# Performance work log

Measured on AMD Instinct MI355X. Metric: run time of the kernel, lower is better.

## Reference

```python
import jax, jax.numpy as jnp
import numpy as np

T, N, E = 4, 50000, 400000
F0, F1, F2 = 128, 128, 64


def _xavier(k, shape):
    a = float(np.sqrt(6.0 / (shape[0] + shape[1])))
    return jax.random.uniform(k, shape, jnp.float32, -a, a)


def setup_inputs() -> dict:
    key = jax.random.key(0)
    ks = jax.random.split(key, 32)
    inp = {
        'node_embs': jax.random.normal(ks[0], (T, N, F0), jnp.float32),
        'mask': jnp.zeros((T, N, 1), jnp.float32),
        'edge_src': jax.random.randint(ks[1], (T, E), 0, N, jnp.int32),
        'edge_dst': jax.random.randint(ks[2], (T, E), 0, N, jnp.int32),
        'edge_weight': jax.random.uniform(ks[3], (T, E), jnp.float32),
        'gcn_w0': _xavier(ks[4], (F0, F1)),
        'gcn_w1': _xavier(ks[5], (F1, F2)),
    }
    i = 6
    for (pre, rows, cols) in (('l0', F0, F1), ('l1', F1, F2)):
        for g in ('u', 'r', 'h'):
            inp[pre + '_W' + g] = _xavier(ks[i], (rows, rows)); i += 1
            inp[pre + '_U' + g] = _xavier(ks[i], (rows, rows)); i += 1
            inp[pre + '_B' + g] = jnp.zeros((rows, cols), jnp.float32)
        inp[pre + '_scorer'] = _xavier(ks[i], (rows, 1)); i += 1
    return inp


def _topk_embed(X, m, scorer, k):
    # scores: [N,1] = X @ scorer / ||scorer|| + mask
    scores = X @ scorer / jnp.linalg.norm(scorer) + m
    vals, idx = jax.lax.top_k(scores[:, 0], k)          # [k]
    return (X[idx] * jnp.tanh(vals)[:, None]).T         # [rows, k]


def _grcu(Q0, params, node_seq, mask_seq, src, dst, ew, k, n_nodes):
    Wu, Uu, Bu, Wr, Ur, Br, Wh, Uh, Bh, scorer = params

    def step(Q, xs):
        X, m, s, d, w = xs
        z = _topk_embed(X, m, scorer, k)                 # [rows, cols]
        upd = jax.nn.sigmoid(Wu @ z + Uu @ Q + Bu)
        rst = jax.nn.sigmoid(Wr @ z + Ur @ Q + Br)
        hcap = jnp.tanh(Wh @ z + Uh @ (rst * Q) + Bh)
        Qn = (1.0 - upd) * Q + upd * hcap                # evolved GCN weight
        XW = X @ Qn                                      # [N, cols]
        msg = XW[s] * w[:, None]                         # gather + scale
        out = jax.nn.relu(jax.ops.segment_sum(msg, d, num_segments=n_nodes))
        return Qn, out

    _, outs = jax.lax.scan(step, Q0, (node_seq, mask_seq, src, dst, ew))
    return outs  # [T, N, cols]


def reference(node_embs, mask, edge_src, edge_dst, edge_weight, gcn_w0, gcn_w1,
              l0_Wu, l0_Uu, l0_Bu, l0_Wr, l0_Ur, l0_Br, l0_Wh, l0_Uh, l0_Bh, l0_scorer,
              l1_Wu, l1_Uu, l1_Bu, l1_Wr, l1_Ur, l1_Br, l1_Wh, l1_Uh, l1_Bh, l1_scorer):
    p0 = (l0_Wu, l0_Uu, l0_Bu, l0_Wr, l0_Ur, l0_Br, l0_Wh, l0_Uh, l0_Bh, l0_scorer)
    p1 = (l1_Wu, l1_Uu, l1_Bu, l1_Wr, l1_Ur, l1_Br, l1_Wh, l1_Uh, l1_Bh, l1_scorer)
    n = node_embs.shape[1]
    h1 = _grcu(gcn_w0, p0, node_embs, mask, edge_src, edge_dst, edge_weight, gcn_w0.shape[1], n)
    h2 = _grcu(gcn_w1, p1, h1, mask, edge_src, edge_dst, edge_weight, gcn_w1.shape[1], n)
    return h2  # [T, N, F2]
```

## Files before the change

kernel.cpp:

```cpp
#include <hip/hip_runtime.h>
#include <math.h>

#define T_STEPS 4
#define NNODES 50000
#define NEDGES 400000
#define FIN 128
#define NBINS 8192
#define BINSHIFT 19
#define EQCAP 4096
#define DSHARD 6250

__device__ __forceinline__ float sigmoidf_(float x) { return 1.0f / (1.0f + __expf(-x)); }

__device__ __forceinline__ unsigned int key_of(float s) {
    unsigned int u = __float_as_uint(s);
    return (u & 0x80000000u) ? ~u : (u | 0x80000000u);
}

__device__ __forceinline__ unsigned short f2bf(float f) {
    unsigned int u = __float_as_uint(f);
    unsigned int r = (u + 0x7FFFu + ((u >> 16) & 1u)) >> 16;
    return (unsigned short)r;
}
__device__ __forceinline__ float bf2f(unsigned short h) {
    return __uint_as_float(((unsigned int)h) << 16);
}

__global__ void norm_kernel(const float* __restrict__ s0, const float* __restrict__ s1,
                            float* __restrict__ norms) {
    __shared__ float red[128];
    int tid = threadIdx.x;
    float a = s0[tid];
    red[tid] = a * a;
    __syncthreads();
    for (int off = 64; off > 0; off >>= 1) { if (tid < off) red[tid] += red[tid + off]; __syncthreads(); }
    if (tid == 0) norms[0] = sqrtf(red[0]);
    __syncthreads();
    float b = s1[tid];
    red[tid] = b * b;
    __syncthreads();
    for (int off = 64; off > 0; off >>= 1) { if (tid < off) red[tid] += red[tid + off]; __syncthreads(); }
    if (tid == 0) norms[1] = sqrtf(red[0]);
}

__global__ void scores_hist4_kernel(const float* __restrict__ node_embs, const float* __restrict__ scorer,
                                    const float* __restrict__ norms,
                                    const float* __restrict__ mask, float* __restrict__ scores4,
                                    int* __restrict__ ghist4, int N) {
    __shared__ float sc[FIN];
    if (threadIdx.x < FIN) sc[threadIdx.x] = scorer[threadIdx.x];
    __syncthreads();
    int t = blockIdx.y;
    int n = blockIdx.x * blockDim.x + threadIdx.x;
    if (n >= N) return;
    const float4* xr = (const float4*)(node_embs + ((size_t)t * N + n) * FIN);
    float acc = 0.f;
#pragma unroll 8
    for (int k4 = 0; k4 < FIN / 4; k4++) {
        float4 v = xr[k4];
        acc += v.x * sc[k4 * 4] + v.y * sc[k4 * 4 + 1] + v.z * sc[k4 * 4 + 2] + v.w * sc[k4 * 4 + 3];
    }
    float s = acc / norms[0] + mask[(size_t)t * N + n];
    scores4[(size_t)t * N + n] = s;
    atomicAdd(&ghist4[t * NBINS + (key_of(s) >> BINSHIFT)], 1);
}

__global__ void __launch_bounds__(256)
topk_collect_kernel(const float* __restrict__ scores_b, const int* __restrict__ ghist_b,
                    int* __restrict__ cnts_b, int* __restrict__ gt_idx_b, float* __restrict__ gt_val_b,
                    int* __restrict__ eq_idx_b, float* __restrict__ eq_val_b, int N, int K) {
    __shared__ int h[NBINS];
    __shared__ int part[256];
    __shared__ int s_bin;
    int tid = threadIdx.x;
    int task = blockIdx.y;
    const int* gh = ghist_b + (size_t)task * NBINS;
    for (int i = tid; i < NBINS; i += 256) h[i] = gh[i];
    __syncthreads();
    int s = 0;
#pragma unroll
    for (int i = 0; i < NBINS / 256; i++) s += h[tid * (NBINS / 256) + i];
    part[tid] = s;
    __syncthreads();
    for (int off = 1; off < 256; off <<= 1) {
        int v = (tid + off < 256) ? part[tid + off] : 0;
        __syncthreads();
        part[tid] += v;
        __syncthreads();
    }
    {
        int run = (tid == 255) ? 0 : part[tid + 1];
        const int CH = NBINS / 256;
        for (int b = tid * CH + CH - 1; b >= tid * CH; b--) {
            int Sb = run + h[b];
            if (Sb >= K && run < K) s_bin = b;
            run = Sb;
        }
    }
    __syncthreads();
    int bin = s_bin;
    const float* scores = scores_b + (size_t)task * N;
    int* cg = cnts_b + task * 2;
    for (int n = blockIdx.x * 256 + tid; n < N; n += gridDim.x * 256) {
        float sc = scores[n];
        unsigned int key = key_of(sc);
        int kb = (int)(key >> BINSHIFT);
        if (kb > bin) {
            int p = atomicAdd(&cg[0], 1);
            gt_idx_b[task * 128 + p] = n; gt_val_b[task * 128 + p] = sc;
        } else if (kb == bin) {
            int p = atomicAdd(&cg[1], 1);
            if (p < EQCAP) { eq_idx_b[task * EQCAP + p] = n; eq_val_b[task * EQCAP + p] = sc; }
        }
    }
}

template <int K>
__global__ void __launch_bounds__(1024)
topk_finish_kernel(int* __restrict__ ghist_b, int* __restrict__ cnts_b,
                   const int* __restrict__ gt_idx_b, const float* __restrict__ gt_val_b,
                   const int* __restrict__ eq_idx_b, const float* __restrict__ eq_val_b,
                   const float* __restrict__ X_b, float* __restrict__ z_b, int N) {
    __shared__ int sidx[K];
    __shared__ float sval[K];
    __shared__ unsigned int ek[EQCAP];
    __shared__ int ei[EQCAP];
    __shared__ int out_idx[K];
    __shared__ float out_tanh[K];
    int tid = threadIdx.x;
    int task = blockIdx.x;
    int* cg = cnts_b + task * 2;
    int g = cg[0];
    int m = min(cg[1], EQCAP);
    int need = K - g;
    const int* gt_idx = gt_idx_b + task * 128;
    const float* gt_val = gt_val_b + task * 128;
    const int* eq_idx = eq_idx_b + task * EQCAP;
    const float* eq_val = eq_val_b + task * EQCAP;
    const float* X = X_b + (size_t)task * N * FIN;
    float* z = z_b + (size_t)task * FIN * K;

    for (int i = tid; i < g; i += 1024) { sidx[i] = gt_idx[i]; sval[i] = gt_val[i]; }
    for (int i = tid; i < m; i += 1024) { ek[i] = key_of(eq_val[i]); ei[i] = eq_idx[i]; }
    __syncthreads();
    for (int i = tid; i < m; i += 1024) {
        int myi = ei[i];
        unsigned int myk = ek[i];
        int rank = 0;
        for (int j = 0; j < m; j++)
            rank += (ek[j] > myk) || (ek[j] == myk && ei[j] < myi);
        if (rank < need) { sidx[g + rank] = myi; sval[g + rank] = eq_val[i]; }
    }
    __syncthreads();
    if (tid < K) {
        float v = sval[tid];
        int id = sidx[tid];
        unsigned int myk = key_of(v);
        int rank = 0;
        for (int j = 0; j < K; j++) {
            unsigned int kj = key_of(sval[j]);
            rank += (kj > myk) || (kj == myk && sidx[j] < id);
        }
        out_idx[rank] = id;
        out_tanh[rank] = tanhf(v);
    }
    int* gh = ghist_b + (size_t)task * NBINS;
    for (int i = tid; i < NBINS; i += 1024) gh[i] = 0;
    if (tid == 0) { cg[0] = 0; cg[1] = 0; }
    __syncthreads();
    for (int i = tid; i < K * FIN; i += 1024) {
        int j = i >> 7;
        int r = i & 127;
        z[r * K + j] = X[(size_t)out_idx[j] * FIN + r] * out_tanh[j];
    }
}

template <int COLS>
__global__ void __launch_bounds__(256)
gru_multi_kernel(const float* __restrict__ Qinit, const float* __restrict__ z_all,
                 const float* __restrict__ Wu, const float* __restrict__ Uu, const float* __restrict__ Bu,
                 const float* __restrict__ Wr, const float* __restrict__ Ur, const float* __restrict__ Br,
                 const float* __restrict__ Wh, const float* __restrict__ Uh, const float* __restrict__ Bh,
                 float* __restrict__ Qn_all) {
    __shared__ float zc[128][8];
    __shared__ float qc[128][8];
    __shared__ float rq[128][8];
    __shared__ float ul[128][8];
    int tid = threadIdx.x;
    int c0 = blockIdx.x * 8;
    for (int i = tid; i < 1024; i += 256) {
        int r = i >> 3, c = i & 7;
        qc[r][c] = Qinit[r * COLS + c0 + c];
    }
    for (int t = 0; t < T_STEPS; t++) {
        __syncthreads();
        const float* z = z_all + (size_t)t * 128 * COLS;
        for (int i = tid; i < 1024; i += 256) {
            int r = i >> 3, c = i & 7;
            zc[r][c] = z[r * COLS + c0 + c];
        }
        __syncthreads();
#pragma unroll
        for (int e = 0; e < 4; e++) {
            int idx = tid + 256 * e;
            int r = idx >> 3, c = idx & 7;
            float au = Bu[r * COLS + c0 + c], ar = Br[r * COLS + c0 + c];
            for (int k = 0; k < 128; k++) {
                float zz = zc[k][c], qq = qc[k][c];
                au += Wu[r * 128 + k] * zz + Uu[r * 128 + k] * qq;
                ar += Wr[r * 128 + k] * zz + Ur[r * 128 + k] * qq;
            }
            ul[r][c] = sigmoidf_(au);
            rq[r][c] = sigmoidf_(ar) * qc[r][c];
        }
        __syncthreads();
        float* Qn = Qn_all + (size_t)t * 128 * COLS;
#pragma unroll
        for (int e = 0; e < 4; e++) {
            int idx = tid + 256 * e;
            int r = idx >> 3, c = idx & 7;
            float s = Bh[r * COLS + c0 + c];
            for (int k = 0; k < 128; k++) {
                s += Wh[r * 128 + k] * zc[k][c] + Uh[r * 128 + k] * rq[k][c];
            }
            float h = tanhf(s);
            float u = ul[r][c];
            float qn = (1.f - u) * qc[r][c] + u * h;
            Qn[r * COLS + c0 + c] = qn;
            qc[r][c] = qn;
        }
    }
}

template <int COLS, bool BF16>
__global__ void __launch_bounds__(256)
xw_kernel(const float* __restrict__ X_b, const float* __restrict__ Qn_all,
          void* __restrict__ outp, int N) {
    constexpr int TPR = COLS / 4;
    constexpr int RPG = 256 / TPR;
    constexpr int RPB = RPG * 4;
    int t = blockIdx.y;
    const float* X = X_b + (size_t)t * N * FIN;
    const float* Qn = Qn_all + (size_t)t * 128 * COLS;
    __shared__ float4 qs[128 * TPR];
    for (int i = threadIdx.x; i < 128 * TPR; i += 256) qs[i] = ((const float4*)Qn)[i];
    __syncthreads();
    int lane_c = threadIdx.x % TPR;
    int rloc = threadIdx.x / TPR;
    int base = blockIdx.x * RPB;
    int rows[4];
    float4 acc[4];
#pragma unroll
    for (int j = 0; j < 4; j++) {
        rows[j] = base + rloc + j * RPG;
        acc[j] = make_float4(0.f, 0.f, 0.f, 0.f);
    }
    int nc[4];
#pragma unroll
    for (int j = 0; j < 4; j++) nc[j] = min(rows[j], N - 1);

    for (int k4 = 0; k4 < 32; k4++) {
        float4 q0 = qs[(k4 * 4 + 0) * TPR + lane_c];
        float4 q1 = qs[(k4 * 4 + 1) * TPR + lane_c];
        float4 q2 = qs[(k4 * 4 + 2) * TPR + lane_c];
        float4 q3 = qs[(k4 * 4 + 3) * TPR + lane_c];
#pragma unroll
        for (int j = 0; j < 4; j++) {
            float4 xv = ((const float4*)(X + (size_t)nc[j] * FIN))[k4];
            acc[j].x += xv.x * q0.x + xv.y * q1.x + xv.z * q2.x + xv.w * q3.x;
            acc[j].y += xv.x * q0.y + xv.y * q1.y + xv.z * q2.y + xv.w * q3.y;
            acc[j].z += xv.x * q0.z + xv.y * q1.z + xv.z * q2.z + xv.w * q3.z;
            acc[j].w += xv.x * q0.w + xv.y * q1.w + xv.z * q2.w + xv.w * q3.w;
        }
    }
#pragma unroll
    for (int j = 0; j < 4; j++) {
        if (rows[j] < N) {
            if (BF16) {
                ushort4 o;
                o.x = f2bf(acc[j].x); o.y = f2bf(acc[j].y);
                o.z = f2bf(acc[j].z); o.w = f2bf(acc[j].w);
                ((ushort4*)((unsigned short*)outp + ((size_t)t * N + rows[j]) * COLS))[lane_c] = o;
            } else {
                ((float4*)((float*)outp + ((size_t)t * N + rows[j]) * COLS))[lane_c] = acc[j];
            }
        }
    }
}

__global__ void hist4_kernel(const int* __restrict__ dst, int* __restrict__ hist4, int E) {
    int e = blockIdx.x * blockDim.x + threadIdx.x;
    if (e >= E) return;
    int t = blockIdx.y;
    atomicAdd(&hist4[t * NNODES + dst[(size_t)t * E + e]], 1);
}

__global__ void __launch_bounds__(256)
scanA_kernel(const int* __restrict__ hist, int* __restrict__ incl, int* __restrict__ bsum, int M) {
    __shared__ int sh[256];
    int gid = blockIdx.x * 256 + threadIdx.x;
    int v = (gid < M) ? hist[gid] : 0;
    sh[threadIdx.x] = v;
    __syncthreads();
    for (int off = 1; off < 256; off <<= 1) {
        int u = (threadIdx.x >= off) ? sh[threadIdx.x - off] : 0;
        __syncthreads();
        sh[threadIdx.x] += u;
        __syncthreads();
    }
    if (gid < M) incl[gid] = sh[threadIdx.x];
    if (threadIdx.x == 255) bsum[blockIdx.x] = sh[255];
}

__global__ void __launch_bounds__(1024)
scanB_kernel(int* __restrict__ bsum, int nb) {
    __shared__ int sh[1024];
    int tid = threadIdx.x;
    int v = (tid < nb) ? bsum[tid] : 0;
    sh[tid] = v;
    __syncthreads();
    for (int off = 1; off < 1024; off <<= 1) {
        int u = (tid >= off) ? sh[tid - off] : 0;
        __syncthreads();
        sh[tid] += u;
        __syncthreads();
    }
    if (tid < nb) bsum[tid] = (tid == 0) ? 0 : sh[tid - 1];
}

__global__ void __launch_bounds__(256)
scanC_kernel(const int* __restrict__ hist, const int* __restrict__ incl,
             const int* __restrict__ bsum, int* __restrict__ row_ptr,
             int* __restrict__ cursor, int M) {
    int gid = blockIdx.x * 256 + threadIdx.x;
    if (gid < M) {
        int inc = incl[gid] + bsum[gid / 256];
        int ex = inc - hist[gid];
        row_ptr[gid] = ex;
        cursor[gid] = ex;
        if (gid == M - 1) row_ptr[M] = inc;
    }
}

__global__ void bucket4_kernel(const int* __restrict__ src, const int* __restrict__ dst,
                               const float* __restrict__ w, int* __restrict__ cursor,
                               int2* __restrict__ sedge, int E) {
    int bx = blockIdx.x;
    int shard = bx & 7;
    int e = (bx >> 3) * 256 + threadIdx.x;
    if (e >= E) return;
    int t = blockIdx.y;
    size_t ge = (size_t)t * E + e;
    int d = dst[ge];
    if (d / DSHARD != shard) return;
    int pos = atomicAdd(&cursor[t * NNODES + d], 1);
    int2 pk;
    pk.x = src[ge];
    pk.y = __float_as_int(w[ge]);
    sedge[pos] = pk;
}

template <int COLS, bool SCORE, bool BF16>
__global__ void __launch_bounds__(256)
agg_kernel(const void* __restrict__ XWp, const int* __restrict__ row_ptr4,
           const int2* __restrict__ sedge,
           float* __restrict__ out_b, int N,
           const float* __restrict__ scorer, const float* __restrict__ norms,
           const float* __restrict__ mask_b, float* __restrict__ scores_b, int* __restrict__ ghist_b) {
    constexpr int TPN = COLS / 4;
    constexpr int NPB = 256 / TPN;
    int t = blockIdx.y;
    int node = blockIdx.x * NPB + threadIdx.x / TPN;
    int lane = threadIdx.x % TPN;
    if (node >= N) return;
    const int* rp = row_ptr4 + (size_t)t * N;
    int beg = rp[node], end = rp[node + 1];
    size_t xwoff = (size_t)t * N * COLS;
    float4 a0 = make_float4(0.f, 0.f, 0.f, 0.f);
    float4 a1 = a0, a2 = a0, a3 = a0;
    int i = beg;
    for (; i + 4 <= end; i += 4) {
        int2 p0 = sedge[i], p1 = sedge[i + 1], p2 = sedge[i + 2], p3 = sedge[i + 3];
        if (BF16) {
            const unsigned short* XW = (const unsigned short*)XWp + xwoff;
            ushort4 v0 = ((const ushort4*)(XW + (size_t)p0.x * COLS))[lane];
            ushort4 v1 = ((const ushort4*)(XW + (size_t)p1.x * COLS))[lane];
            ushort4 v2 = ((const ushort4*)(XW + (size_t)p2.x * COLS))[lane];
            ushort4 v3 = ((const ushort4*)(XW + (size_t)p3.x * COLS))[lane];
            float w0 = __int_as_float(p0.y), w1 = __int_as_float(p1.y);
            float w2 = __int_as_float(p2.y), w3 = __int_as_float(p3.y);
            a0.x += bf2f(v0.x) * w0; a0.y += bf2f(v0.y) * w0; a0.z += bf2f(v0.z) * w0; a0.w += bf2f(v0.w) * w0;
            a1.x += bf2f(v1.x) * w1; a1.y += bf2f(v1.y) * w1; a1.z += bf2f(v1.z) * w1; a1.w += bf2f(v1.w) * w1;
            a2.x += bf2f(v2.x) * w2; a2.y += bf2f(v2.y) * w2; a2.z += bf2f(v2.z) * w2; a2.w += bf2f(v2.w) * w2;
            a3.x += bf2f(v3.x) * w3; a3.y += bf2f(v3.y) * w3; a3.z += bf2f(v3.z) * w3; a3.w += bf2f(v3.w) * w3;
        } else {
            const float* XW = (const float*)XWp + xwoff;
            float4 v0 = ((const float4*)(XW + (size_t)p0.x * COLS))[lane];
            float4 v1 = ((const float4*)(XW + (size_t)p1.x * COLS))[lane];
            float4 v2 = ((const float4*)(XW + (size_t)p2.x * COLS))[lane];
            float4 v3 = ((const float4*)(XW + (size_t)p3.x * COLS))[lane];
            float w0 = __int_as_float(p0.y), w1 = __int_as_float(p1.y);
            float w2 = __int_as_float(p2.y), w3 = __int_as_float(p3.y);
            a0.x += v0.x * w0; a0.y += v0.y * w0; a0.z += v0.z * w0; a0.w += v0.w * w0;
            a1.x += v1.x * w1; a1.y += v1.y * w1; a1.z += v1.z * w1; a1.w += v1.w * w1;
            a2.x += v2.x * w2; a2.y += v2.y * w2; a2.z += v2.z * w2; a2.w += v2.w * w2;
            a3.x += v3.x * w3; a3.y += v3.y * w3; a3.z += v3.z * w3; a3.w += v3.w * w3;
        }
    }
    for (; i < end; i++) {
        int2 pk = sedge[i];
        float wt = __int_as_float(pk.y);
        if (BF16) {
            const unsigned short* XW = (const unsigned short*)XWp + xwoff;
            ushort4 v = ((const ushort4*)(XW + (size_t)pk.x * COLS))[lane];
            a0.x += bf2f(v.x) * wt; a0.y += bf2f(v.y) * wt;
            a0.z += bf2f(v.z) * wt; a0.w += bf2f(v.w) * wt;
        } else {
            const float* XW = (const float*)XWp + xwoff;
            float4 v = ((const float4*)(XW + (size_t)pk.x * COLS))[lane];
            a0.x += v.x * wt; a0.y += v.y * wt; a0.z += v.z * wt; a0.w += v.w * wt;
        }
    }
    float4 acc;
    acc.x = (a0.x + a1.x) + (a2.x + a3.x);
    acc.y = (a0.y + a1.y) + (a2.y + a3.y);
    acc.z = (a0.z + a1.z) + (a2.z + a3.z);
    acc.w = (a0.w + a1.w) + (a2.w + a3.w);
    acc.x = fmaxf(acc.x, 0.f); acc.y = fmaxf(acc.y, 0.f);
    acc.z = fmaxf(acc.z, 0.f); acc.w = fmaxf(acc.w, 0.f);
    ((float4*)(out_b + ((size_t)t * N + node) * COLS))[lane] = acc;
    if (SCORE) {
        float4 sc4 = ((const float4*)scorer)[lane];
        float partial = acc.x * sc4.x + acc.y * sc4.y + acc.z * sc4.z + acc.w * sc4.w;
#pragma unroll
        for (int off = TPN / 2; off > 0; off >>= 1) partial += __shfl_xor(partial, off, TPN);
        if (lane == 0) {
            float s = partial / norms[1] + mask_b[(size_t)t * N + node];
            scores_b[(size_t)t * N + node] = s;
            atomicAdd(&ghist_b[t * NBINS + (key_of(s) >> BINSHIFT)], 1);
        }
    }
}

extern "C" void kernel_launch(void* const* d_in, const int* in_sizes, int n_in,
                              void* d_out, int out_size, void* d_ws, size_t ws_size,
                              hipStream_t stream) {
    const float* node_embs   = (const float*)d_in[0];
    const float* mask        = (const float*)d_in[1];
    const int*   edge_src    = (const int*)d_in[2];
    const int*   edge_dst    = (const int*)d_in[3];
    const float* edge_weight = (const float*)d_in[4];
    const float* gcn_w0      = (const float*)d_in[5];
    const float* gcn_w1      = (const float*)d_in[6];
    const float* l0p[10];
    const float* l1p[10];
    for (int i = 0; i < 10; i++) l0p[i] = (const float*)d_in[7 + i];
    for (int i = 0; i < 10; i++) l1p[i] = (const float*)d_in[17 + i];

    char* ws = (char*)d_ws;
    size_t off = 0;
    auto alloc = [&](size_t bytes) -> void* {
        void* p = ws + off;
        off += (bytes + 255) / 256 * 256;
        return p;
    };
    float* XW0buf = (float*)alloc((size_t)4 * NNODES * 128 * 4);
    float* h1buf  = (float*)alloc((size_t)4 * NNODES * 128 * 4);
    unsigned short* XW1buf = (unsigned short*)alloc((size_t)4 * NNODES * 64 * 2);
    float* scores4= (float*)alloc((size_t)4 * NNODES * 4);
    float* scores1= (float*)alloc((size_t)4 * NNODES * 4);
    float* z0buf  = (float*)alloc((size_t)4 * 128 * 128 * 4);
    float* z1buf  = (float*)alloc((size_t)4 * 128 * 64 * 4);
    float* Q0n    = (float*)alloc((size_t)4 * 128 * 128 * 4);
    float* Q1n    = (float*)alloc((size_t)4 * 128 * 64 * 4);
    float* norms  = (float*)alloc(64);
    int* hist4    = (int*)alloc(((size_t)4 * NNODES + 8 * NBINS + 64) * 4);
    int* ghist0   = hist4 + 4 * NNODES;
    int* ghist1   = ghist0 + 4 * NBINS;
    int* cnts     = ghist1 + 4 * NBINS;
    int* incl4    = (int*)alloc((size_t)4 * NNODES * 4);
    int* bsumb    = (int*)alloc(1024 * 4);
    int* rowp4    = (int*)alloc(((size_t)4 * NNODES + 1) * 4);
    int* cursor4  = (int*)alloc((size_t)4 * NNODES * 4);
    int2* sedge4  = (int2*)alloc((size_t)4 * NEDGES * 8);
    int*   gt_idx = (int*)alloc((size_t)4 * 128 * 4);
    float* gt_val = (float*)alloc((size_t)4 * 128 * 4);
    int*   eq_idx = (int*)alloc((size_t)4 * EQCAP * 4);
    float* eq_val = (float*)alloc((size_t)4 * EQCAP * 4);

    hipMemsetAsync(hist4, 0, ((size_t)4 * NNODES + 8 * NBINS + 64) * 4, stream);
    norm_kernel<<<1, 128, 0, stream>>>(l0p[9], l1p[9], norms);

    const int M4 = 4 * NNODES;
    const int NB4 = (M4 + 255) / 256;
    const int NB = (NNODES + 255) / 256;
    const int EB = (NEDGES + 255) / 256;

    hist4_kernel<<<dim3(EB, 4), 256, 0, stream>>>(edge_dst, hist4, NEDGES);
    scanA_kernel<<<NB4, 256, 0, stream>>>(hist4, incl4, bsumb, M4);
    scanB_kernel<<<1, 1024, 0, stream>>>(bsumb, NB4);
    scanC_kernel<<<NB4, 256, 0, stream>>>(hist4, incl4, bsumb, rowp4, cursor4, M4);
    bucket4_kernel<<<dim3(EB * 8, 4), 256, 0, stream>>>(edge_src, edge_dst, edge_weight, cursor4, sedge4, NEDGES);

    scores_hist4_kernel<<<dim3(NB, 4), 256, 0, stream>>>(node_embs, l0p[9], norms, mask, scores4, ghist0, NNODES);
    topk_collect_kernel<<<dim3(NB, 4), 256, 0, stream>>>(scores4, ghist0, cnts, gt_idx, gt_val, eq_idx, eq_val, NNODES, 128);
    topk_finish_kernel<128><<<4, 1024, 0, stream>>>(ghist0, cnts, gt_idx, gt_val, eq_idx, eq_val, node_embs, z0buf, NNODES);

    gru_multi_kernel<128><<<16, 256, 0, stream>>>(gcn_w0, z0buf,
        l0p[0], l0p[1], l0p[2], l0p[3], l0p[4], l0p[5], l0p[6], l0p[7], l0p[8], Q0n);
    xw_kernel<128, false><<<dim3((NNODES + 31) / 32, 4), 256, 0, stream>>>(node_embs, Q0n, XW0buf, NNODES);
    agg_kernel<128, true, false><<<dim3((NNODES + 7) / 8, 4), 256, 0, stream>>>(XW0buf, rowp4, sedge4, h1buf, NNODES,
        l1p[9], norms, mask, scores1, ghist1);

    topk_collect_kernel<<<dim3(NB, 4), 256, 0, stream>>>(scores1, ghist1, cnts, gt_idx, gt_val, eq_idx, eq_val, NNODES, 64);
    topk_finish_kernel<64><<<4, 1024, 0, stream>>>(ghist1, cnts, gt_idx, gt_val, eq_idx, eq_val, h1buf, z1buf, NNODES);
    gru_multi_kernel<64><<<8, 256, 0, stream>>>(gcn_w1, z1buf,
        l1p[0], l1p[1], l1p[2], l1p[3], l1p[4], l1p[5], l1p[6], l1p[7], l1p[8], Q1n);
    xw_kernel<64, true><<<dim3((NNODES + 63) / 64, 4), 256, 0, stream>>>(h1buf, Q1n, XW1buf, NNODES);
    agg_kernel<64, false, true><<<dim3((NNODES + 15) / 16, 4), 256, 0, stream>>>(XW1buf, rowp4, sedge4, (float*)d_out, NNODES,
        nullptr, nullptr, nullptr, nullptr, nullptr);
}
```

Baseline: 1.229 ms.

## Shard CSR edges by source range and map aggregation blocks to XCDs

Edges for each (timestep, destination) are now grouped into 8 source-range shards, using a larger histogram and a two-level prefix scan. The aggregation kernel walks the shards in order, with a block barrier after each one, so concurrently running blocks gather from the same slice of XW and that slice can stay resident in L2. Block indices are also remapped so that each pair of XCDs works on a single timestep. The cost is an 8x larger histogram, scan and cursor workspace, an extra scan pass, per-shard loop overhead and barriers, and very short per-shard edge runs that mostly fall into the non-unrolled tail loop.

```diff
diff --git a/kernel.cpp b/kernel.cpp
--- a/kernel.cpp
+++ b/kernel.cpp
@@ -288,11 +288,14 @@
     }
 }
 
-__global__ void hist4_kernel(const int* __restrict__ dst, int* __restrict__ hist4, int E) {
+__global__ void hist8_kernel(const int* __restrict__ src, const int* __restrict__ dst,
+                             int* __restrict__ hist8, int E) {
     int e = blockIdx.x * blockDim.x + threadIdx.x;
     if (e >= E) return;
     int t = blockIdx.y;
-    atomicAdd(&hist4[t * NNODES + dst[(size_t)t * E + e]], 1);
+    size_t ge = (size_t)t * E + e;
+    int s = src[ge] / DSHARD;
+    atomicAdd(&hist8[(t * 8 + s) * NNODES + dst[ge]], 1);
 }
 
 __global__ void __launch_bounds__(256)
@@ -329,12 +332,15 @@
 }
 
 __global__ void __launch_bounds__(256)
-scanC_kernel(const int* __restrict__ hist, const int* __restrict__ incl,
-             const int* __restrict__ bsum, int* __restrict__ row_ptr,
-             int* __restrict__ cursor, int M) {
+scanC2_kernel(const int* __restrict__ hist, const int* __restrict__ inclA,
+              const int* __restrict__ bsumA, const int* __restrict__ inclB,
+              const int* __restrict__ bsumB, int* __restrict__ row_ptr,
+              int* __restrict__ cursor, int M) {
     int gid = blockIdx.x * 256 + threadIdx.x;
     if (gid < M) {
-        int inc = incl[gid] + bsum[gid / 256];
+        int b = gid >> 8;
+        int exBlock = inclB[b] - bsumA[b] + bsumB[b >> 8];
+        int inc = inclA[gid] + exBlock;
         int ex = inc - hist[gid];
         row_ptr[gid] = ex;
         cursor[gid] = ex;
@@ -342,7 +348,7 @@
     }
 }
 
-__global__ void bucket4_kernel(const int* __restrict__ src, const int* __restrict__ dst,
+__global__ void bucket8_kernel(const int* __restrict__ src, const int* __restrict__ dst,
                                const float* __restrict__ w, int* __restrict__ cursor,
                                int2* __restrict__ sedge, int E) {
     int bx = blockIdx.x;
@@ -351,75 +357,85 @@
     if (e >= E) return;
     int t = blockIdx.y;
     size_t ge = (size_t)t * E + e;
+    int sc = src[ge];
+    if (sc / DSHARD != shard) return;
     int d = dst[ge];
-    if (d / DSHARD != shard) return;
-    int pos = atomicAdd(&cursor[t * NNODES + d], 1);
+    int pos = atomicAdd(&cursor[(t * 8 + shard) * NNODES + d], 1);
     int2 pk;
-    pk.x = src[ge];
+    pk.x = sc;
     pk.y = __float_as_int(w[ge]);
     sedge[pos] = pk;
 }
 
 template <int COLS, bool SCORE, bool BF16>
 __global__ void __launch_bounds__(256)
-agg_kernel(const void* __restrict__ XWp, const int* __restrict__ row_ptr4,
+agg_kernel(const void* __restrict__ XWp, const int* __restrict__ rp8,
            const int2* __restrict__ sedge,
            float* __restrict__ out_b, int N,
            const float* __restrict__ scorer, const float* __restrict__ norms,
            const float* __restrict__ mask_b, float* __restrict__ scores_b, int* __restrict__ ghist_b) {
     constexpr int TPN = COLS / 4;
     constexpr int NPB = 256 / TPN;
-    int t = blockIdx.y;
-    int node = blockIdx.x * NPB + threadIdx.x / TPN;
+    int lin = blockIdx.x;
+    int xcd = lin & 7;
+    int slot = lin >> 3;
+    int t = xcd >> 1;
+    int db = slot * 2 + (xcd & 1);
+    int dstBlocks = (N + NPB - 1) / NPB;
+    if (db >= dstBlocks) return;
+    int node = db * NPB + threadIdx.x / TPN;
     int lane = threadIdx.x % TPN;
-    if (node >= N) return;
-    const int* rp = row_ptr4 + (size_t)t * N;
-    int beg = rp[node], end = rp[node + 1];
     size_t xwoff = (size_t)t * N * COLS;
     float4 a0 = make_float4(0.f, 0.f, 0.f, 0.f);
     float4 a1 = a0, a2 = a0, a3 = a0;
-    int i = beg;
-    for (; i + 4 <= end; i += 4) {
-        int2 p0 = sedge[i], p1 = sedge[i + 1], p2 = sedge[i + 2], p3 = sedge[i + 3];
-        if (BF16) {
-            const unsigned short* XW = (const unsigned short*)XWp + xwoff;
-            ushort4 v0 = ((const ushort4*)(XW + (size_t)p0.x * COLS))[lane];
-            ushort4 v1 = ((const ushort4*)(XW + (size_t)p1.x * COLS))[lane];
-            ushort4 v2 = ((const ushort4*)(XW + (size_t)p2.x * COLS))[lane];
-            ushort4 v3 = ((const ushort4*)(XW + (size_t)p3.x * COLS))[lane];
-            float w0 = __int_as_float(p0.y), w1 = __int_as_float(p1.y);
-            float w2 = __int_as_float(p2.y), w3 = __int_as_float(p3.y);
-            a0.x += bf2f(v0.x) * w0; a0.y += bf2f(v0.y) * w0; a0.z += bf2f(v0.z) * w0; a0.w += bf2f(v0.w) * w0;
-            a1.x += bf2f(v1.x) * w1; a1.y += bf2f(v1.y) * w1; a1.z += bf2f(v1.z) * w1; a1.w += bf2f(v1.w) * w1;
-            a2.x += bf2f(v2.x) * w2; a2.y += bf2f(v2.y) * w2; a2.z += bf2f(v2.z) * w2; a2.w += bf2f(v2.w) * w2;
-            a3.x += bf2f(v3.x) * w3; a3.y += bf2f(v3.y) * w3; a3.z += bf2f(v3.z) * w3; a3.w += bf2f(v3.w) * w3;
-        } else {
-            const float* XW = (const float*)XWp + xwoff;
-            float4 v0 = ((const float4*)(XW + (size_t)p0.x * COLS))[lane];
-            float4 v1 = ((const float4*)(XW + (size_t)p1.x * COLS))[lane];
-            float4 v2 = ((const float4*)(XW + (size_t)p2.x * COLS))[lane];
-            float4 v3 = ((const float4*)(XW + (size_t)p3.x * COLS))[lane];
-            float w0 = __int_as_float(p0.y), w1 = __int_as_float(p1.y);
-            float w2 = __int_as_float(p2.y), w3 = __int_as_float(p3.y);
-            a0.x += v0.x * w0; a0.y += v0.y * w0; a0.z += v0.z * w0; a0.w += v0.w * w0;
-            a1.x += v1.x * w1; a1.y += v1.y * w1; a1.z += v1.z * w1; a1.w += v1.w * w1;
-            a2.x += v2.x * w2; a2.y += v2.y * w2; a2.z += v2.z * w2; a2.w += v2.w * w2;
-            a3.x += v3.x * w3; a3.y += v3.y * w3; a3.z += v3.z * w3; a3.w += v3.w * w3;
-        }
-    }
-    for (; i < end; i++) {
-        int2 pk = sedge[i];
-        float wt = __int_as_float(pk.y);
-        if (BF16) {
-            const unsigned short* XW = (const unsigned short*)XWp + xwoff;
-            ushort4 v = ((const ushort4*)(XW + (size_t)pk.x * COLS))[lane];
-            a0.x += bf2f(v.x) * wt; a0.y += bf2f(v.y) * wt;
-            a0.z += bf2f(v.z) * wt; a0.w += bf2f(v.w) * wt;
-        } else {
-            const float* XW = (const float*)XWp + xwoff;
-            float4 v = ((const float4*)(XW + (size_t)pk.x * COLS))[lane];
-            a0.x += v.x * wt; a0.y += v.y * wt; a0.z += v.z * wt; a0.w += v.w * wt;
-        }
+#pragma unroll 1
+    for (int s = 0; s < 8; s++) {
+        size_t ridx = (size_t)(t * 8 + s) * N + node;
+        int i = rp8[ridx];
+        int end = rp8[ridx + 1];
+        for (; i + 4 <= end; i += 4) {
+            int2 p0 = sedge[i], p1 = sedge[i + 1], p2 = sedge[i + 2], p3 = sedge[i + 3];
+            if (BF16) {
+                const unsigned short* XW = (const unsigned short*)XWp + xwoff;
+                ushort4 v0 = ((const ushort4*)(XW + (size_t)p0.x * COLS))[lane];
+                ushort4 v1 = ((const ushort4*)(XW + (size_t)p1.x * COLS))[lane];
+                ushort4 v2 = ((const ushort4*)(XW + (size_t)p2.x * COLS))[lane];
+                ushort4 v3 = ((const ushort4*)(XW + (size_t)p3.x * COLS))[lane];
+                float w0 = __int_as_float(p0.y), w1 = __int_as_float(p1.y);
+                float w2 = __int_as_float(p2.y), w3 = __int_as_float(p3.y);
+                a0.x += bf2f(v0.x) * w0; a0.y += bf2f(v0.y) * w0; a0.z += bf2f(v0.z) * w0; a0.w += bf2f(v0.w) * w0;
+                a1.x += bf2f(v1.x) * w1; a1.y += bf2f(v1.y) * w1; a1.z += bf2f(v1.z) * w1; a1.w += bf2f(v1.w) * w1;
+                a2.x += bf2f(v2.x) * w2; a2.y += bf2f(v2.y) * w2; a2.z += bf2f(v2.z) * w2; a2.w += bf2f(v2.w) * w2;
+                a3.x += bf2f(v3.x) * w3; a3.y += bf2f(v3.y) * w3; a3.z += bf2f(v3.z) * w3; a3.w += bf2f(v3.w) * w3;
+            } else {
+                const float* XW = (const float*)XWp + xwoff;
+                float4 v0 = ((const float4*)(XW + (size_t)p0.x * COLS))[lane];
+                float4 v1 = ((const float4*)(XW + (size_t)p1.x * COLS))[lane];
+                float4 v2 = ((const float4*)(XW + (size_t)p2.x * COLS))[lane];
+                float4 v3 = ((const float4*)(XW + (size_t)p3.x * COLS))[lane];
+                float w0 = __int_as_float(p0.y), w1 = __int_as_float(p1.y);
+                float w2 = __int_as_float(p2.y), w3 = __int_as_float(p3.y);
+                a0.x += v0.x * w0; a0.y += v0.y * w0; a0.z += v0.z * w0; a0.w += v0.w * w0;
+                a1.x += v1.x * w1; a1.y += v1.y * w1; a1.z += v1.z * w1; a1.w += v1.w * w1;
+                a2.x += v2.x * w2; a2.y += v2.y * w2; a2.z += v2.z * w2; a2.w += v2.w * w2;
+                a3.x += v3.x * w3; a3.y += v3.y * w3; a3.z += v3.z * w3; a3.w += v3.w * w3;
+            }
+        }
+        for (; i < end; i++) {
+            int2 pk = sedge[i];
+            float wt = __int_as_float(pk.y);
+            if (BF16) {
+                const unsigned short* XW = (const unsigned short*)XWp + xwoff;
+                ushort4 v = ((const ushort4*)(XW + (size_t)pk.x * COLS))[lane];
+                a0.x += bf2f(v.x) * wt; a0.y += bf2f(v.y) * wt;
+                a0.z += bf2f(v.z) * wt; a0.w += bf2f(v.w) * wt;
+            } else {
+                const float* XW = (const float*)XWp + xwoff;
+                float4 v = ((const float4*)(XW + (size_t)pk.x * COLS))[lane];
+                a0.x += v.x * wt; a0.y += v.y * wt; a0.z += v.z * wt; a0.w += v.w * wt;
+            }
+        }
+        __syncthreads();
     }
     float4 acc;
     acc.x = (a0.x + a1.x) + (a2.x + a3.x);
@@ -474,33 +490,37 @@
     float* Q0n    = (float*)alloc((size_t)4 * 128 * 128 * 4);
     float* Q1n    = (float*)alloc((size_t)4 * 128 * 64 * 4);
     float* norms  = (float*)alloc(64);
-    int* hist4    = (int*)alloc(((size_t)4 * NNODES + 8 * NBINS + 64) * 4);
-    int* ghist0   = hist4 + 4 * NNODES;
+    const int M8 = 32 * NNODES;
+    int* hist8    = (int*)alloc(((size_t)M8 + 8 * NBINS + 64) * 4);
+    int* ghist0   = hist8 + M8;
     int* ghist1   = ghist0 + 4 * NBINS;
     int* cnts     = ghist1 + 4 * NBINS;
-    int* incl4    = (int*)alloc((size_t)4 * NNODES * 4);
-    int* bsumb    = (int*)alloc(1024 * 4);
-    int* rowp4    = (int*)alloc(((size_t)4 * NNODES + 1) * 4);
-    int* cursor4  = (int*)alloc((size_t)4 * NNODES * 4);
+    int* inclA    = (int*)alloc((size_t)M8 * 4);
+    int* bsumA    = (int*)alloc(8192 * 4);
+    int* inclB    = (int*)alloc(8192 * 4);
+    int* bsumB    = (int*)alloc(1024 * 4);
+    int* rowp8    = (int*)alloc(((size_t)M8 + 1) * 4);
+    int* cursor8  = (int*)alloc((size_t)M8 * 4);
     int2* sedge4  = (int2*)alloc((size_t)4 * NEDGES * 8);
     int*   gt_idx = (int*)alloc((size_t)4 * 128 * 4);
     float* gt_val = (float*)alloc((size_t)4 * 128 * 4);
     int*   eq_idx = (int*)alloc((size_t)4 * EQCAP * 4);
     float* eq_val = (float*)alloc((size_t)4 * EQCAP * 4);
 
-    hipMemsetAsync(hist4, 0, ((size_t)4 * NNODES + 8 * NBINS + 64) * 4, stream);
+    hipMemsetAsync(hist8, 0, ((size_t)M8 + 8 * NBINS + 64) * 4, stream);
     norm_kernel<<<1, 128, 0, stream>>>(l0p[9], l1p[9], norms);
 
-    const int M4 = 4 * NNODES;
-    const int NB4 = (M4 + 255) / 256;
     const int NB = (NNODES + 255) / 256;
     const int EB = (NEDGES + 255) / 256;
-
-    hist4_kernel<<<dim3(EB, 4), 256, 0, stream>>>(edge_dst, hist4, NEDGES);
-    scanA_kernel<<<NB4, 256, 0, stream>>>(hist4, incl4, bsumb, M4);
-    scanB_kernel<<<1, 1024, 0, stream>>>(bsumb, NB4);
-    scanC_kernel<<<NB4, 256, 0, stream>>>(hist4, incl4, bsumb, rowp4, cursor4, M4);
-    bucket4_kernel<<<dim3(EB * 8, 4), 256, 0, stream>>>(edge_src, edge_dst, edge_weight, cursor4, sedge4, NEDGES);
+    const int NB8  = (M8 + 255) / 256;
+    const int NB8b = (NB8 + 255) / 256;
+
+    hist8_kernel<<<dim3(EB, 4), 256, 0, stream>>>(edge_src, edge_dst, hist8, NEDGES);
+    scanA_kernel<<<NB8, 256, 0, stream>>>(hist8, inclA, bsumA, M8);
+    scanA_kernel<<<NB8b, 256, 0, stream>>>(bsumA, inclB, bsumB, NB8);
+    scanB_kernel<<<1, 1024, 0, stream>>>(bsumB, NB8b);
+    scanC2_kernel<<<NB8, 256, 0, stream>>>(hist8, inclA, bsumA, inclB, bsumB, rowp8, cursor8, M8);
+    bucket8_kernel<<<dim3(EB * 8, 4), 256, 0, stream>>>(edge_src, edge_dst, edge_weight, cursor8, sedge4, NEDGES);
 
     scores_hist4_kernel<<<dim3(NB, 4), 256, 0, stream>>>(node_embs, l0p[9], norms, mask, scores4, ghist0, NNODES);
     topk_collect_kernel<<<dim3(NB, 4), 256, 0, stream>>>(scores4, ghist0, cnts, gt_idx, gt_val, eq_idx, eq_val, NNODES, 128);
@@ -509,14 +529,22 @@
     gru_multi_kernel<128><<<16, 256, 0, stream>>>(gcn_w0, z0buf,
         l0p[0], l0p[1], l0p[2], l0p[3], l0p[4], l0p[5], l0p[6], l0p[7], l0p[8], Q0n);
     xw_kernel<128, false><<<dim3((NNODES + 31) / 32, 4), 256, 0, stream>>>(node_embs, Q0n, XW0buf, NNODES);
-    agg_kernel<128, true, false><<<dim3((NNODES + 7) / 8, 4), 256, 0, stream>>>(XW0buf, rowp4, sedge4, h1buf, NNODES,
-        l1p[9], norms, mask, scores1, ghist1);
+    {
+        const int dstBlocks0 = (NNODES + 7) / 8;
+        const int grid0 = ((dstBlocks0 + 1) / 2) * 8;
+        agg_kernel<128, true, false><<<grid0, 256, 0, stream>>>(XW0buf, rowp8, sedge4, h1buf, NNODES,
+            l1p[9], norms, mask, scores1, ghist1);
+    }
 
     topk_collect_kernel<<<dim3(NB, 4), 256, 0, stream>>>(scores1, ghist1, cnts, gt_idx, gt_val, eq_idx, eq_val, NNODES, 64);
     topk_finish_kernel<64><<<4, 1024, 0, stream>>>(ghist1, cnts, gt_idx, gt_val, eq_idx, eq_val, h1buf, z1buf, NNODES);
     gru_multi_kernel<64><<<8, 256, 0, stream>>>(gcn_w1, z1buf,
         l1p[0], l1p[1], l1p[2], l1p[3], l1p[4], l1p[5], l1p[6], l1p[7], l1p[8], Q1n);
     xw_kernel<64, true><<<dim3((NNODES + 63) / 64, 4), 256, 0, stream>>>(h1buf, Q1n, XW1buf, NNODES);
-    agg_kernel<64, false, true><<<dim3((NNODES + 15) / 16, 4), 256, 0, stream>>>(XW1buf, rowp4, sedge4, (float*)d_out, NNODES,
-        nullptr, nullptr, nullptr, nullptr, nullptr);
-}
+    {
+        const int dstBlocks1 = (NNODES + 15) / 16;
+        const int grid1 = ((dstBlocks1 + 1) / 2) * 8;
+        agg_kernel<64, false, true><<<grid1, 256, 0, stream>>>(XW1buf, rowp8, sedge4, (float*)d_out, NNODES,
+            nullptr, nullptr, nullptr, nullptr, nullptr);
+    }
+}
```

Result: slower. 1.324 ms (+7.7%).

## Split layer-0 aggregation into column-slice passes with XCD-aware block mapping

Applied to the files above, without the earlier changes.

The layer-0 gather-aggregate runs as four passes, each over a 32-column slice of XW, so the gathered working set per pass (50000×32 floats per timestep) is more likely to stay cache-resident. Partial scorer dot products carry across passes in a new scoreacc buffer. Both aggregation kernels remap the flat block index so each XCD (index mod 8) handles one timestep's half of the destinations, keeping that timestep's XW in that XCD's L2. Outputs use nontemporal stores. The cost is re-reading the CSR edge list four times and three extra launches.

```diff
diff --git a/kernel.cpp b/kernel.cpp
--- a/kernel.cpp
+++ b/kernel.cpp
@@ -24,6 +24,12 @@
 }
 __device__ __forceinline__ float bf2f(unsigned short h) {
     return __uint_as_float(((unsigned int)h) << 16);
+}
+
+typedef float f4v __attribute__((ext_vector_type(4)));
+__device__ __forceinline__ void nt_store4(float* p, float4 v) {
+    f4v w; w.x = v.x; w.y = v.y; w.z = v.z; w.w = v.w;
+    __builtin_nontemporal_store(w, (f4v*)p);
 }
 
 __global__ void norm_kernel(const float* __restrict__ s0, const float* __restrict__ s1,
@@ -360,66 +366,51 @@
     sedge[pos] = pk;
 }
 
-template <int COLS, bool SCORE, bool BF16>
-__global__ void __launch_bounds__(256)
-agg_kernel(const void* __restrict__ XWp, const int* __restrict__ row_ptr4,
-           const int2* __restrict__ sedge,
-           float* __restrict__ out_b, int N,
-           const float* __restrict__ scorer, const float* __restrict__ norms,
-           const float* __restrict__ mask_b, float* __restrict__ scores_b, int* __restrict__ ghist_b) {
-    constexpr int TPN = COLS / 4;
+template <int SW, bool SCORE>
+__global__ void __launch_bounds__(256)
+agg_slice_kernel(const float* __restrict__ XW_b, const int* __restrict__ row_ptr4,
+                 const int2* __restrict__ sedge,
+                 float* __restrict__ out_b, int N, int P,
+                 const float* __restrict__ scorer, const float* __restrict__ norms,
+                 const float* __restrict__ mask_b, float* __restrict__ scores_b,
+                 int* __restrict__ ghist_b, float* __restrict__ scoreacc) {
+    constexpr int TPN = SW / 4;
     constexpr int NPB = 256 / TPN;
-    int t = blockIdx.y;
-    int node = blockIdx.x * NPB + threadIdx.x / TPN;
+    constexpr int NPASS = FIN / SW;
+    int lin = blockIdx.x;
+    int xcd = lin & 7;
+    int slot = lin >> 3;
+    int t = xcd >> 1;
+    int db = slot * 2 + (xcd & 1);
+    int dstBlocks = (N + NPB - 1) / NPB;
+    if (db >= dstBlocks) return;
+    int node = db * NPB + threadIdx.x / TPN;
+    if (node >= N) return;
     int lane = threadIdx.x % TPN;
-    if (node >= N) return;
     const int* rp = row_ptr4 + (size_t)t * N;
     int beg = rp[node], end = rp[node + 1];
-    size_t xwoff = (size_t)t * N * COLS;
+    const float* XW = XW_b + (size_t)t * N * FIN + P * SW;
     float4 a0 = make_float4(0.f, 0.f, 0.f, 0.f);
     float4 a1 = a0, a2 = a0, a3 = a0;
     int i = beg;
     for (; i + 4 <= end; i += 4) {
         int2 p0 = sedge[i], p1 = sedge[i + 1], p2 = sedge[i + 2], p3 = sedge[i + 3];
-        if (BF16) {
-            const unsigned short* XW = (const unsigned short*)XWp + xwoff;
-            ushort4 v0 = ((const ushort4*)(XW + (size_t)p0.x * COLS))[lane];
-            ushort4 v1 = ((const ushort4*)(XW + (size_t)p1.x * COLS))[lane];
-            ushort4 v2 = ((const ushort4*)(XW + (size_t)p2.x * COLS))[lane];
-            ushort4 v3 = ((const ushort4*)(XW + (size_t)p3.x * COLS))[lane];
-            float w0 = __int_as_float(p0.y), w1 = __int_as_float(p1.y);
-            float w2 = __int_as_float(p2.y), w3 = __int_as_float(p3.y);
-            a0.x += bf2f(v0.x) * w0; a0.y += bf2f(v0.y) * w0; a0.z += bf2f(v0.z) * w0; a0.w += bf2f(v0.w) * w0;
-            a1.x += bf2f(v1.x) * w1; a1.y += bf2f(v1.y) * w1; a1.z += bf2f(v1.z) * w1; a1.w += bf2f(v1.w) * w1;
-            a2.x += bf2f(v2.x) * w2; a2.y += bf2f(v2.y) * w2; a2.z += bf2f(v2.z) * w2; a2.w += bf2f(v2.w) * w2;
-            a3.x += bf2f(v3.x) * w3; a3.y += bf2f(v3.y) * w3; a3.z += bf2f(v3.z) * w3; a3.w += bf2f(v3.w) * w3;
-        } else {
-            const float* XW = (const float*)XWp + xwoff;
-            float4 v0 = ((const float4*)(XW + (size_t)p0.x * COLS))[lane];
-            float4 v1 = ((const float4*)(XW + (size_t)p1.x * COLS))[lane];
-            float4 v2 = ((const float4*)(XW + (size_t)p2.x * COLS))[lane];
-            float4 v3 = ((const float4*)(XW + (size_t)p3.x * COLS))[lane];
-            float w0 = __int_as_float(p0.y), w1 = __int_as_float(p1.y);
-            float w2 = __int_as_float(p2.y), w3 = __int_as_float(p3.y);
-            a0.x += v0.x * w0; a0.y += v0.y * w0; a0.z += v0.z * w0; a0.w += v0.w * w0;
-            a1.x += v1.x * w1; a1.y += v1.y * w1; a1.z += v1.z * w1; a1.w += v1.w * w1;
-            a2.x += v2.x * w2; a2.y += v2.y * w2; a2.z += v2.z * w2; a2.w += v2.w * w2;
-            a3.x += v3.x * w3; a3.y += v3.y * w3; a3.z += v3.z * w3; a3.w += v3.w * w3;
-        }
+        float4 v0 = ((const float4*)(XW + (size_t)p0.x * FIN))[lane];
+        float4 v1 = ((const float4*)(XW + (size_t)p1.x * FIN))[lane];
+        float4 v2 = ((const float4*)(XW + (size_t)p2.x * FIN))[lane];
+        float4 v3 = ((const float4*)(XW + (size_t)p3.x * FIN))[lane];
+        float w0 = __int_as_float(p0.y), w1 = __int_as_float(p1.y);
+        float w2 = __int_as_float(p2.y), w3 = __int_as_float(p3.y);
+        a0.x += v0.x * w0; a0.y += v0.y * w0; a0.z += v0.z * w0; a0.w += v0.w * w0;
+        a1.x += v1.x * w1; a1.y += v1.y * w1; a1.z += v1.z * w1; a1.w += v1.w * w1;
+        a2.x += v2.x * w2; a2.y += v2.y * w2; a2.z += v2.z * w2; a2.w += v2.w * w2;
+        a3.x += v3.x * w3; a3.y += v3.y * w3; a3.z += v3.z * w3; a3.w += v3.w * w3;
     }
     for (; i < end; i++) {
         int2 pk = sedge[i];
         float wt = __int_as_float(pk.y);
-        if (BF16) {
-            const unsigned short* XW = (const unsigned short*)XWp + xwoff;
-            ushort4 v = ((const ushort4*)(XW + (size_t)pk.x * COLS))[lane];
-            a0.x += bf2f(v.x) * wt; a0.y += bf2f(v.y) * wt;
-            a0.z += bf2f(v.z) * wt; a0.w += bf2f(v.w) * wt;
-        } else {
-            const float* XW = (const float*)XWp + xwoff;
-            float4 v = ((const float4*)(XW + (size_t)pk.x * COLS))[lane];
-            a0.x += v.x * wt; a0.y += v.y * wt; a0.z += v.z * wt; a0.w += v.w * wt;
-        }
+        float4 v = ((const float4*)(XW + (size_t)pk.x * FIN))[lane];
+        a0.x += v.x * wt; a0.y += v.y * wt; a0.z += v.z * wt; a0.w += v.w * wt;
     }
     float4 acc;
     acc.x = (a0.x + a1.x) + (a2.x + a3.x);
@@ -428,18 +419,77 @@
     acc.w = (a0.w + a1.w) + (a2.w + a3.w);
     acc.x = fmaxf(acc.x, 0.f); acc.y = fmaxf(acc.y, 0.f);
     acc.z = fmaxf(acc.z, 0.f); acc.w = fmaxf(acc.w, 0.f);
-    ((float4*)(out_b + ((size_t)t * N + node) * COLS))[lane] = acc;
+    nt_store4(out_b + ((size_t)t * N + node) * FIN + P * SW + lane * 4, acc);
     if (SCORE) {
-        float4 sc4 = ((const float4*)scorer)[lane];
+        float4 sc4 = ((const float4*)(scorer + P * SW))[lane];
         float partial = acc.x * sc4.x + acc.y * sc4.y + acc.z * sc4.z + acc.w * sc4.w;
 #pragma unroll
         for (int off = TPN / 2; off > 0; off >>= 1) partial += __shfl_xor(partial, off, TPN);
         if (lane == 0) {
-            float s = partial / norms[1] + mask_b[(size_t)t * N + node];
-            scores_b[(size_t)t * N + node] = s;
-            atomicAdd(&ghist_b[t * NBINS + (key_of(s) >> BINSHIFT)], 1);
-        }
-    }
+            float* sa = scoreacc + (size_t)t * N + node;
+            float tot = (P == 0 ? 0.f : *sa) + partial;
+            if (P == NPASS - 1) {
+                float s = tot / norms[1] + mask_b[(size_t)t * N + node];
+                scores_b[(size_t)t * N + node] = s;
+                atomicAdd(&ghist_b[t * NBINS + (key_of(s) >> BINSHIFT)], 1);
+            } else {
+                *sa = tot;
+            }
+        }
+    }
+}
+
+template <int COLS>
+__global__ void __launch_bounds__(256)
+agg_kernel(const unsigned short* __restrict__ XWb, const int* __restrict__ row_ptr4,
+           const int2* __restrict__ sedge,
+           float* __restrict__ out_b, int N) {
+    constexpr int TPN = COLS / 4;
+    constexpr int NPB = 256 / TPN;
+    int lin = blockIdx.x;
+    int xcd = lin & 7;
+    int slot = lin >> 3;
+    int t = xcd >> 1;
+    int db = slot * 2 + (xcd & 1);
+    int dstBlocks = (N + NPB - 1) / NPB;
+    if (db >= dstBlocks) return;
+    int node = db * NPB + threadIdx.x / TPN;
+    if (node >= N) return;
+    int lane = threadIdx.x % TPN;
+    const int* rp = row_ptr4 + (size_t)t * N;
+    int beg = rp[node], end = rp[node + 1];
+    const unsigned short* XW = XWb + (size_t)t * N * COLS;
+    float4 a0 = make_float4(0.f, 0.f, 0.f, 0.f);
+    float4 a1 = a0, a2 = a0, a3 = a0;
+    int i = beg;
+    for (; i + 4 <= end; i += 4) {
+        int2 p0 = sedge[i], p1 = sedge[i + 1], p2 = sedge[i + 2], p3 = sedge[i + 3];
+        ushort4 v0 = ((const ushort4*)(XW + (size_t)p0.x * COLS))[lane];
+        ushort4 v1 = ((const ushort4*)(XW + (size_t)p1.x * COLS))[lane];
+        ushort4 v2 = ((const ushort4*)(XW + (size_t)p2.x * COLS))[lane];
+        ushort4 v3 = ((const ushort4*)(XW + (size_t)p3.x * COLS))[lane];
+        float w0 = __int_as_float(p0.y), w1 = __int_as_float(p1.y);
+        float w2 = __int_as_float(p2.y), w3 = __int_as_float(p3.y);
+        a0.x += bf2f(v0.x) * w0; a0.y += bf2f(v0.y) * w0; a0.z += bf2f(v0.z) * w0; a0.w += bf2f(v0.w) * w0;
+        a1.x += bf2f(v1.x) * w1; a1.y += bf2f(v1.y) * w1; a1.z += bf2f(v1.z) * w1; a1.w += bf2f(v1.w) * w1;
+        a2.x += bf2f(v2.x) * w2; a2.y += bf2f(v2.y) * w2; a2.z += bf2f(v2.z) * w2; a2.w += bf2f(v2.w) * w2;
+        a3.x += bf2f(v3.x) * w3; a3.y += bf2f(v3.y) * w3; a3.z += bf2f(v3.z) * w3; a3.w += bf2f(v3.w) * w3;
+    }
+    for (; i < end; i++) {
+        int2 pk = sedge[i];
+        float wt = __int_as_float(pk.y);
+        ushort4 v = ((const ushort4*)(XW + (size_t)pk.x * COLS))[lane];
+        a0.x += bf2f(v.x) * wt; a0.y += bf2f(v.y) * wt;
+        a0.z += bf2f(v.z) * wt; a0.w += bf2f(v.w) * wt;
+    }
+    float4 acc;
+    acc.x = (a0.x + a1.x) + (a2.x + a3.x);
+    acc.y = (a0.y + a1.y) + (a2.y + a3.y);
+    acc.z = (a0.z + a1.z) + (a2.z + a3.z);
+    acc.w = (a0.w + a1.w) + (a2.w + a3.w);
+    acc.x = fmaxf(acc.x, 0.f); acc.y = fmaxf(acc.y, 0.f);
+    acc.z = fmaxf(acc.z, 0.f); acc.w = fmaxf(acc.w, 0.f);
+    nt_store4(out_b + ((size_t)t * N + node) * COLS + lane * 4, acc);
 }
 
 extern "C" void kernel_launch(void* const* d_in, const int* in_sizes, int n_in,
@@ -469,6 +519,7 @@
     unsigned short* XW1buf = (unsigned short*)alloc((size_t)4 * NNODES * 64 * 2);
     float* scores4= (float*)alloc((size_t)4 * NNODES * 4);
     float* scores1= (float*)alloc((size_t)4 * NNODES * 4);
+    float* scoreacc=(float*)alloc((size_t)4 * NNODES * 4);
     float* z0buf  = (float*)alloc((size_t)4 * 128 * 128 * 4);
     float* z1buf  = (float*)alloc((size_t)4 * 128 * 64 * 4);
     float* Q0n    = (float*)alloc((size_t)4 * 128 * 128 * 4);
@@ -509,14 +560,23 @@
     gru_multi_kernel<128><<<16, 256, 0, stream>>>(gcn_w0, z0buf,
         l0p[0], l0p[1], l0p[2], l0p[3], l0p[4], l0p[5], l0p[6], l0p[7], l0p[8], Q0n);
     xw_kernel<128, false><<<dim3((NNODES + 31) / 32, 4), 256, 0, stream>>>(node_embs, Q0n, XW0buf, NNODES);
-    agg_kernel<128, true, false><<<dim3((NNODES + 7) / 8, 4), 256, 0, stream>>>(XW0buf, rowp4, sedge4, h1buf, NNODES,
-        l1p[9], norms, mask, scores1, ghist1);
+    {
+        const int dstBlocksS = (NNODES + 31) / 32;
+        const int gridS = ((dstBlocksS + 1) / 2) * 8;
+        for (int P = 0; P < 4; P++) {
+            agg_slice_kernel<32, true><<<gridS, 256, 0, stream>>>(XW0buf, rowp4, sedge4, h1buf, NNODES, P,
+                l1p[9], norms, mask, scores1, ghist1, scoreacc);
+        }
+    }
 
     topk_collect_kernel<<<dim3(NB, 4), 256, 0, stream>>>(scores1, ghist1, cnts, gt_idx, gt_val, eq_idx, eq_val, NNODES, 64);
     topk_finish_kernel<64><<<4, 1024, 0, stream>>>(ghist1, cnts, gt_idx, gt_val, eq_idx, eq_val, h1buf, z1buf, NNODES);
     gru_multi_kernel<64><<<8, 256, 0, stream>>>(gcn_w1, z1buf,
         l1p[0], l1p[1], l1p[2], l1p[3], l1p[4], l1p[5], l1p[6], l1p[7], l1p[8], Q1n);
     xw_kernel<64, true><<<dim3((NNODES + 63) / 64, 4), 256, 0, stream>>>(h1buf, Q1n, XW1buf, NNODES);
-    agg_kernel<64, false, true><<<dim3((NNODES + 15) / 16, 4), 256, 0, stream>>>(XW1buf, rowp4, sedge4, (float*)d_out, NNODES,
-        nullptr, nullptr, nullptr, nullptr, nullptr);
-}
+    {
+        const int dstBlocks1 = (NNODES + 15) / 16;
+        const int grid1 = ((dstBlocks1 + 1) / 2) * 8;
+        agg_kernel<64><<<grid1, 256, 0, stream>>>(XW1buf, rowp4, sedge4, (float*)d_out, NNODES);
+    }
+}
```

New measurement: 1.191 ms. 3.1% less time.
